# Kernel optimization log

Hardware: AMD Instinct MI355X
Metric: run time of the kernel (lower is better)

The kernel has to match this reference:

```python
import jax, jax.numpy as jnp
import numpy as np

B, S, D, H = 8, 1024, 1024, 16
HD = D // H  # head dim = 64


def setup_inputs() -> dict:
    key = jax.random.key(0)
    ks = jax.random.split(key, 8)
    return {
        "hidden_states": jax.random.normal(ks[0], (B, S, D), dtype=jnp.float32),
        "attention_mask": jnp.zeros((B, 1, 1, S), dtype=jnp.float32),
        "Wq": jax.random.normal(ks[1], (D, D), dtype=jnp.float32) * (1.0 / np.sqrt(D)),
        "bq": jax.random.normal(ks[2], (D,), dtype=jnp.float32) * 0.02,
        "Wk": jax.random.normal(ks[3], (D, D), dtype=jnp.float32) * (1.0 / np.sqrt(D)),
        "bk": jax.random.normal(ks[4], (D,), dtype=jnp.float32) * 0.02,
        "Wv": jax.random.normal(ks[5], (D, D), dtype=jnp.float32) * (1.0 / np.sqrt(D)),
        "bv": jax.random.normal(ks[6], (D,), dtype=jnp.float32) * 0.02,
    }


def _split_heads(x):
    # [B,S,D] -> [B,H,S,HD]
    return x.reshape(B, S, H, HD).transpose(0, 2, 1, 3)


def reference(hidden_states, attention_mask, Wq, bq, Wk, bk, Wv, bv):
    q = _split_heads(hidden_states @ Wq + bq)
    k = _split_heads(hidden_states @ Wk + bk)
    v = _split_heads(hidden_states @ Wv + bv)
    # [B,H,S,S]
    scores = jnp.einsum("bhqd,bhkd->bhqk", q, k) / jnp.sqrt(jnp.float32(HD))
    scores = scores + attention_mask
    probs = jax.nn.softmax(scores, axis=-1)  # dropout p=0.0 (eval)
    ctx = jnp.einsum("bhqk,bhkd->bhqd", probs, v)
    # [B,H,S,HD] -> [B,S,D]
    return ctx.transpose(0, 2, 1, 3).reshape(B, S, D)
```

## Files before the change

### kernel.cpp

```cpp
#include <hip/hip_runtime.h>
#include <stdint.h>

#define BB 8
#define SS 1024
#define DD 1024
#define HH 16
#define HDIM 64

typedef __bf16 bf16x8 __attribute__((ext_vector_type(8)));
typedef float f32x4 __attribute__((ext_vector_type(4)));

__device__ __forceinline__ unsigned short f2bf(float f) {
    union { float f; unsigned u; } v; v.f = f;
    unsigned r = v.u + 0x7fff + ((v.u >> 16) & 1);
    return (unsigned short)(r >> 16);
}

__device__ __forceinline__ float exp2fast(float x) {
#if __has_builtin(__builtin_amdgcn_exp2f)
    return __builtin_amdgcn_exp2f(x);
#else
    return __expf(x * 0.69314718f);
#endif
}

__device__ __forceinline__ void async16(void* lds, const void* g) {
    __builtin_amdgcn_global_load_lds(
        (const __attribute__((address_space(1))) unsigned int*)g,
        (__attribute__((address_space(3))) unsigned int*)lds, 16, 0, 0);
}

__global__ __launch_bounds__(256) void prep(
    const float* __restrict__ x, unsigned short* __restrict__ xb,
    const float* __restrict__ w0, const float* __restrict__ w1,
    const float* __restrict__ w2,
    unsigned short* __restrict__ f0, unsigned short* __restrict__ f1,
    unsigned short* __restrict__ f2)
{
    int bid = blockIdx.x;
    int tid = threadIdx.x;
    if (bid < 4096) {
        size_t base = ((size_t)bid << 11) + tid * 8;
        float4 v0 = *reinterpret_cast<const float4*>(x + base);
        float4 v1 = *reinterpret_cast<const float4*>(x + base + 4);
        union { unsigned short u16[8]; uint4 v; } o;
        o.u16[0] = f2bf(v0.x); o.u16[1] = f2bf(v0.y);
        o.u16[2] = f2bf(v0.z); o.u16[3] = f2bf(v0.w);
        o.u16[4] = f2bf(v1.x); o.u16[5] = f2bf(v1.y);
        o.u16[6] = f2bf(v1.z); o.u16[7] = f2bf(v1.w);
        *reinterpret_cast<uint4*>(xb + base) = o.v;
        return;
    }
    __shared__ unsigned short tile[64 * 76];
    int idx = bid - 4096;
    int z = idx >> 8, rem = idx & 255;
    const float* w = (z == 0) ? w0 : (z == 1) ? w1 : w2;
    unsigned short* wf = (z == 0) ? f0 : (z == 1) ? f1 : f2;
    int kt = rem & 15, nt = rem >> 4;
    const float* src = w + (size_t)(kt * 64) * DD + nt * 64;
    #pragma unroll
    for (int i = 0; i < 4; ++i) {
        int f = tid + i * 256;
        int r = f >> 4, c4 = f & 15;
        float4 v = *reinterpret_cast<const float4*>(src + r * DD + c4 * 4);
        ushort4 o;
        o.x = f2bf(v.x); o.y = f2bf(v.y); o.z = f2bf(v.z); o.w = f2bf(v.w);
        *reinterpret_cast<ushort4*>(&tile[r * 76 + c4 * 4]) = o;
    }
    __syncthreads();
    #pragma unroll
    for (int i = 0; i < 2; ++i) {
        int s = tid + i * 256;
        int r = s >> 3, c8 = s & 7;
        unsigned short tmp[8];
        #pragma unroll
        for (int j = 0; j < 8; ++j) tmp[j] = tile[(c8 * 8 + j) * 76 + r];
        *reinterpret_cast<uint4*>(wf + (size_t)(nt * 64 + r) * DD + kt * 64 + c8 * 8) =
            *reinterpret_cast<const uint4*>(tmp);
    }
}

__global__ __launch_bounds__(256, 2) void gemm_qkv(
    const unsigned short* __restrict__ xb,
    const unsigned short* __restrict__ wt0, const unsigned short* __restrict__ wt1,
    const unsigned short* __restrict__ wt2,
    const float* __restrict__ b0, const float* __restrict__ b1, const float* __restrict__ b2,
    unsigned short* __restrict__ qo, unsigned short* __restrict__ ko,
    unsigned short* __restrict__ vto)
{
    __shared__ unsigned short SH[32768];

    int bid = blockIdx.x;
    int xcd = bid & 7, g = bid >> 3;
    int strip = xcd * 3 + (g % 3);
    int mt = g / 3;
    int nt = strip & 7, z = strip >> 3;

    const unsigned short* wt; const float* bias; unsigned short* out;
    if (z == 0)      { wt = wt0; bias = b0; out = qo; }
    else if (z == 1) { wt = wt1; bias = b1; out = ko; }
    else             { wt = wt2; bias = b2; out = vto; }

    int tid = threadIdx.x;
    int wave = tid >> 6, lane = tid & 63, lq = lane >> 4, lm = lane & 15;
    int wr = wave >> 1, wc = wave & 1;

    const unsigned short* sA[4]; const unsigned short* sB[4];
    int dOff[4];
    #pragma unroll
    for (int s = 0; s < 4; ++s) {
        int o = tid + s * 256;
        int rw = o >> 3, cs = o & 7;
        int cl = (cs - rw) & 7;
        dOff[s] = o * 8;
        sA[s] = xb + (size_t)(mt * 128 + rw) * DD + cl * 8;
        sB[s] = wt + (size_t)(nt * 128 + rw) * DD + cl * 8;
    }

#define STAGE(P, KT)                                                          \
    {                                                                         \
        _Pragma("unroll") for (int s_ = 0; s_ < 4; ++s_)                      \
            async16(&SH[(P) * 8192 + dOff[s_]], sA[s_] + (KT) * 64);          \
        _Pragma("unroll") for (int s_ = 0; s_ < 4; ++s_)                      \
            async16(&SH[16384 + (P) * 8192 + dOff[s_]], sB[s_] + (KT) * 64);  \
    }

    int rA[4][2], rB[4][2];
    #pragma unroll
    for (int i = 0; i < 4; ++i) {
        int rwA = wr * 64 + i * 16 + lm;
        int rwB = wc * 64 + i * 16 + lm;
        #pragma unroll
        for (int ks = 0; ks < 2; ++ks) {
            rA[i][ks] = rwA * 64 + (((ks * 4 + lq) + rwA) & 7) * 8;
            rB[i][ks] = rwB * 64 + (((ks * 4 + lq) + rwB) & 7) * 8;
        }
    }

    f32x4 acc[4][4] = {};

#define COMPUTE(P)                                                            \
    {                                                                         \
        const unsigned short* Abuf = &SH[(P) * 8192];                         \
        const unsigned short* Bbuf = &SH[16384 + (P) * 8192];                 \
        _Pragma("unroll") for (int ks_ = 0; ks_ < 2; ++ks_) {                 \
            bf16x8 af[4], bf[4];                                              \
            _Pragma("unroll") for (int i_ = 0; i_ < 4; ++i_)                  \
                af[i_] = *reinterpret_cast<const bf16x8*>(Abuf + rA[i_][ks_]);\
            _Pragma("unroll") for (int j_ = 0; j_ < 4; ++j_)                  \
                bf[j_] = *reinterpret_cast<const bf16x8*>(Bbuf + rB[j_][ks_]);\
            _Pragma("unroll") for (int i_ = 0; i_ < 4; ++i_)                  \
                _Pragma("unroll") for (int j_ = 0; j_ < 4; ++j_)              \
                    acc[i_][j_] = __builtin_amdgcn_mfma_f32_16x16x32_bf16(    \
                        af[i_], bf[j_], acc[i_][j_], 0, 0, 0);                \
        }                                                                     \
    }

    STAGE(0, 0);
    STAGE(1, 1);

    for (int kt = 0; kt < 14; ++kt) {
        int p = kt & 1;
        asm volatile("s_waitcnt vmcnt(8)" ::: "memory");
        __builtin_amdgcn_s_barrier();
        __builtin_amdgcn_sched_barrier(0);
        COMPUTE(p);
        asm volatile("s_waitcnt lgkmcnt(0)" ::: "memory");
        __builtin_amdgcn_sched_barrier(0);
        __builtin_amdgcn_s_barrier();
        STAGE(p, kt + 2);
    }
    asm volatile("s_waitcnt vmcnt(8)" ::: "memory");
    __builtin_amdgcn_s_barrier();
    __builtin_amdgcn_sched_barrier(0);
    COMPUTE(0);
    asm volatile("s_waitcnt vmcnt(0)" ::: "memory");
    __builtin_amdgcn_s_barrier();
    __builtin_amdgcn_sched_barrier(0);
    COMPUTE(1);
#undef STAGE
#undef COMPUTE

    __syncthreads();

    int m0 = mt * 128;
    int col0 = nt * 128 + wc * 64;
    if (z == 2) {
        #pragma unroll
        for (int j = 0; j < 4; ++j) {
            int col = col0 + j * 16 + lm;
            float bsv = bias[col];
            int h = col >> 6, hd = col & 63;
            #pragma unroll
            for (int i = 0; i < 4; ++i) {
                int m = m0 + wr * 64 + i * 16 + lq * 4;
                int b_ = m >> 10, sr = m & 1023;
                union { float f; unsigned u; } p0, p1, p2, p3;
                p0.f = acc[i][j][0] + bsv; p1.f = acc[i][j][1] + bsv;
                p2.f = acc[i][j][2] + bsv; p3.f = acc[i][j][3] + bsv;
                uint2 pk;
                pk.x = __builtin_amdgcn_perm(p1.u + 0x8000u, p0.u + 0x8000u, 0x07060302u);
                pk.y = __builtin_amdgcn_perm(p3.u + 0x8000u, p2.u + 0x8000u, 0x07060302u);
                *reinterpret_cast<uint2*>(out + (((b_ * HH + h) * HDIM + hd) << 10) + sr) = pk;
            }
        }
    } else {
        unsigned short* S = SH + wave * 4864;
        #pragma unroll
        for (int j = 0; j < 4; ++j) {
            float bsv = bias[col0 + j * 16 + lm];
            #pragma unroll
            for (int i = 0; i < 4; ++i) {
                #pragma unroll
                for (int r = 0; r < 4; ++r) {
                    union { float f; unsigned u; } cv; cv.f = acc[i][j][r] + bsv;
                    S[(i * 16 + lq * 4 + r) * 76 + j * 16 + lm] =
                        (unsigned short)((cv.u + 0x8000u) >> 16);
                }
            }
        }
        int h = col0 >> 6;
        int mrow = m0 + wr * 64;
        int b_ = mrow >> 10, sr0 = mrow & 1023;
        unsigned short* ob = out + ((size_t)((b_ * HH + h) << 10) + sr0) * HDIM;
        #pragma unroll
        for (int u = 0; u < 8; ++u) {
            int s = lane + u * 64;
            int row = s >> 3, c8 = s & 7;
            uint4 v = *reinterpret_cast<const uint4*>(&S[row * 76 + c8 * 8]);
            *reinterpret_cast<uint4*>(ob + row * HDIM + c8 * 8) = v;
        }
    }
}

__global__ __launch_bounds__(256, 4) void attention(
    const unsigned short* __restrict__ q,
    const unsigned short* __restrict__ k,
    const unsigned short* __restrict__ vt,
    const float* __restrict__ mask,
    float* __restrict__ out)
{
    __shared__ unsigned short Ks[2][64 * 64];
    __shared__ unsigned short Vs[2][64 * 64];
    __shared__ unsigned short Ps[4][16 * 64];

    int blk = blockIdx.x;
    int xcd = blk & 7, j = blk >> 3;
    int bh = (xcd << 4) + (j >> 3);
    int qt = j & 7;
    int b = bh >> 4, h = bh & 15;

    int tid = threadIdx.x;
    int wave = tid >> 6, lane = tid & 63, lq = lane >> 4, lm = lane & 15;

    const unsigned short* qp = q + (size_t)bh * SS * HDIM;
    const unsigned short* kp = k + (size_t)bh * SS * HDIM;
    const unsigned short* vp = vt + (size_t)bh * HDIM * SS;
    const float* maskb = mask + b * SS;

    int qbase = qt * 128 + wave * 16 + lm;
    bf16x8 qa00 = *reinterpret_cast<const bf16x8*>(qp + qbase * HDIM + lq * 8);
    bf16x8 qa01 = *reinterpret_cast<const bf16x8*>(qp + qbase * HDIM + 32 + lq * 8);
    bf16x8 qa10 = *reinterpret_cast<const bf16x8*>(qp + (qbase + 64) * HDIM + lq * 8);
    bf16x8 qa11 = *reinterpret_cast<const bf16x8*>(qp + (qbase + 64) * HDIM + 32 + lq * 8);

    float lsum0 = 0.f, lsum1 = 0.f;
    f32x4 o0[4] = {}, o1[4] = {};

    int row0 = tid >> 3, sg = tid & 7;
    int cg = (sg - row0) & 7;
    const unsigned short* gk = kp + row0 * 64 + cg * 8;
    const unsigned short* gv = vp + row0 * SS + cg * 8;

    int sl0 = ((lq + lm) & 7) * 8;
    int sl1 = ((lq + lm + 4) & 7) * 8;
    unsigned short* Pw = Ps[wave];
    int pwbase = lm * 64 + (lq & 1) * 4;
    int prd0 = lm * 64 + sl0;
    int prd1 = lm * 64 + sl1;

    async16(&Ks[0][tid * 8], gk);  async16(&Ks[0][(tid + 256) * 8], gk + 32 * 64);
    async16(&Vs[0][tid * 8], gv);  async16(&Vs[0][(tid + 256) * 8], gv + 32 * SS);
    gk += 64 * 64; gv += 64;

    for (int t = 0; t < 16; ++t) {
        int p = t & 1;
        __syncthreads();
        int kb0 = t * 64;

        float4 mk[4];
        #pragma unroll
        for (int nb = 0; nb < 4; ++nb) {
            mk[nb] = *reinterpret_cast<const float4*>(maskb + kb0 + nb * 16 + lq * 4);
            #pragma unroll
            for (int r = 0; r < 4; ++r)
                reinterpret_cast<float*>(&mk[nb])[r] *= 1.44269504f;
        }
        if (t < 15) {
            async16(&Ks[p ^ 1][tid * 8], gk);  async16(&Ks[p ^ 1][(tid + 256) * 8], gk + 32 * 64);
            async16(&Vs[p ^ 1][tid * 8], gv);  async16(&Vs[p ^ 1][(tid + 256) * 8], gv + 32 * SS);
            gk += 64 * 64; gv += 64;
        }

        f32x4 c0[4], c1[4];
        #pragma unroll
        for (int nb = 0; nb < 4; ++nb) {
            bf16x8 kf0 = *reinterpret_cast<const bf16x8*>(&Ks[p][(nb * 16 + lm) * 64 + sl0]);
            bf16x8 kf1 = *reinterpret_cast<const bf16x8*>(&Ks[p][(nb * 16 + lm) * 64 + sl1]);
            f32x4 z = {};
            z = __builtin_amdgcn_mfma_f32_16x16x32_bf16(kf0, qa00, z, 0, 0, 0);
            z = __builtin_amdgcn_mfma_f32_16x16x32_bf16(kf1, qa01, z, 0, 0, 0);
            c0[nb] = z;
            f32x4 w = {};
            w = __builtin_amdgcn_mfma_f32_16x16x32_bf16(kf0, qa10, w, 0, 0, 0);
            w = __builtin_amdgcn_mfma_f32_16x16x32_bf16(kf1, qa11, w, 0, 0, 0);
            c1[nb] = w;
        }

        #pragma unroll
        for (int nb = 0; nb < 4; ++nb) {
            unsigned u[4];
            #pragma unroll
            for (int r = 0; r < 4; ++r) {
                float e = exp2fast(fmaf(c0[nb][r], 0.18033688f,
                                        reinterpret_cast<const float*>(&mk[nb])[r]));
                union { float f; unsigned v; } cv; cv.f = e;
                u[r] = cv.v;
                union { unsigned v; float f; } tr; tr.v = cv.v & 0xffff0000u;
                lsum0 += tr.f;
            }
            uint2 pk;
            pk.x = __builtin_amdgcn_perm(u[1], u[0], 0x07060302u);
            pk.y = __builtin_amdgcn_perm(u[3], u[2], 0x07060302u);
            *reinterpret_cast<uint2*>(
                &Pw[pwbase + (((nb * 2 + (lq >> 1)) + lm) & 7) * 8]) = pk;
        }
        bf16x8 pa00 = *reinterpret_cast<const bf16x8*>(&Pw[prd0]);
        bf16x8 pa01 = *reinterpret_cast<const bf16x8*>(&Pw[prd1]);

        #pragma unroll
        for (int nb = 0; nb < 4; ++nb) {
            unsigned u[4];
            #pragma unroll
            for (int r = 0; r < 4; ++r) {
                float e = exp2fast(fmaf(c1[nb][r], 0.18033688f,
                                        reinterpret_cast<const float*>(&mk[nb])[r]));
                union { float f; unsigned v; } cv; cv.f = e;
                u[r] = cv.v;
                union { unsigned v; float f; } tr; tr.v = cv.v & 0xffff0000u;
                lsum1 += tr.f;
            }
            uint2 pk;
            pk.x = __builtin_amdgcn_perm(u[1], u[0], 0x07060302u);
            pk.y = __builtin_amdgcn_perm(u[3], u[2], 0x07060302u);
            *reinterpret_cast<uint2*>(
                &Pw[pwbase + (((nb * 2 + (lq >> 1)) + lm) & 7) * 8]) = pk;
        }
        bf16x8 pa10 = *reinterpret_cast<const bf16x8*>(&Pw[prd0]);
        bf16x8 pa11 = *reinterpret_cast<const bf16x8*>(&Pw[prd1]);

        #pragma unroll
        for (int nb2 = 0; nb2 < 4; ++nb2) {
            bf16x8 vf0 = *reinterpret_cast<const bf16x8*>(&Vs[p][(nb2 * 16 + lm) * 64 + sl0]);
            o0[nb2] = __builtin_amdgcn_mfma_f32_16x16x32_bf16(pa00, vf0, o0[nb2], 0, 0, 0);
            o1[nb2] = __builtin_amdgcn_mfma_f32_16x16x32_bf16(pa10, vf0, o1[nb2], 0, 0, 0);
            bf16x8 vf1 = *reinterpret_cast<const bf16x8*>(&Vs[p][(nb2 * 16 + lm) * 64 + sl1]);
            o0[nb2] = __builtin_amdgcn_mfma_f32_16x16x32_bf16(pa01, vf1, o0[nb2], 0, 0, 0);
            o1[nb2] = __builtin_amdgcn_mfma_f32_16x16x32_bf16(pa11, vf1, o1[nb2], 0, 0, 0);
        }
    }

    lsum0 += __shfl_xor(lsum0, 16, 64);
    lsum0 += __shfl_xor(lsum0, 32, 64);
    lsum1 += __shfl_xor(lsum1, 16, 64);
    lsum1 += __shfl_xor(lsum1, 32, 64);
    float linv0[4], linv1[4];
    #pragma unroll
    for (int r = 0; r < 4; ++r) {
        linv0[r] = 1.0f / __shfl(lsum0, lq * 4 + r, 64);
        linv1[r] = 1.0f / __shfl(lsum1, lq * 4 + r, 64);
    }

    int srb = qt * 128 + wave * 16;
    #pragma unroll
    for (int nb2 = 0; nb2 < 4; ++nb2) {
        #pragma unroll
        for (int r = 0; r < 4; ++r) {
            int sr = srb + lq * 4 + r;
            out[((size_t)(b * SS + sr)) * DD + h * HDIM + nb2 * 16 + lm] =
                o0[nb2][r] * linv0[r];
            out[((size_t)(b * SS + sr + 64)) * DD + h * HDIM + nb2 * 16 + lm] =
                o1[nb2][r] * linv1[r];
        }
    }
}

extern "C" void kernel_launch(void* const* d_in, const int* in_sizes, int n_in,
                              void* d_out, int out_size, void* d_ws, size_t ws_size,
                              hipStream_t stream) {
    const float* hs   = (const float*)d_in[0];
    const float* mask = (const float*)d_in[1];
    const float* Wq   = (const float*)d_in[2];
    const float* bq   = (const float*)d_in[3];
    const float* Wk   = (const float*)d_in[4];
    const float* bk   = (const float*)d_in[5];
    const float* Wv   = (const float*)d_in[6];
    const float* bv   = (const float*)d_in[7];
    float* out = (float*)d_out;

    char* ws = (char*)d_ws;
    unsigned short* XB  = (unsigned short*)(ws);
    unsigned short* WT0 = (unsigned short*)(ws + 16777216);
    unsigned short* WT1 = (unsigned short*)(ws + 18874368);
    unsigned short* WT2 = (unsigned short*)(ws + 20971520);
    unsigned short* qw  = (unsigned short*)(ws + 23068672);
    unsigned short* kw  = (unsigned short*)(ws + 39845888);
    unsigned short* vtw = (unsigned short*)(ws + 56623104);

    prep<<<4864, 256, 0, stream>>>(hs, XB, Wq, Wk, Wv, WT0, WT1, WT2);
    gemm_qkv<<<1536, 256, 0, stream>>>(XB, WT0, WT1, WT2,
                                       bq, bk, bv, qw, kw, vtw);
    attention<<<1024, 256, 0, stream>>>(qw, kw, vtw, mask, out);
}
```

Baseline: 216.8 us.

## Enlarge QKV GEMM tile to 256x128 with 8 waves and software-pipelined LDS reads

The QKV projection GEMM moves from 256-thread 128x128 tiles to 512-thread 256x128 tiles, halving the grid and sharing each staged B tile across twice as many rows. The inner loop is split into quadrant steps: LDS fragment reads for the next quadrant are double-buffered in registers and overlap MFMA work. The next global-to-LDS stage is issued mid-tile, and wave priority is raised around MFMA bursts. The aim is less global and LDS traffic per FLOP and less stall between LDS reads and matrix ops. The cost is more barriers, higher register and LDS use (96 KB) with one block per CU, and fewer blocks to balance across CUs.

```diff
diff --git a/kernel.cpp b/kernel.cpp
--- a/kernel.cpp
+++ b/kernel.cpp
@@ -29,6 +29,15 @@
         (const __attribute__((address_space(1))) unsigned int*)g,
         (__attribute__((address_space(3))) unsigned int*)lds, 16, 0, 0);
 }
+
+#define WAITVM6 asm volatile("s_waitcnt vmcnt(6)" ::: "memory")
+#define WAITVM0 asm volatile("s_waitcnt vmcnt(0)" ::: "memory")
+#define WAITLG8 asm volatile("s_waitcnt lgkmcnt(8)" ::: "memory")
+#define WAITLG0 asm volatile("s_waitcnt lgkmcnt(0)" ::: "memory")
+#define SB0 __builtin_amdgcn_sched_barrier(0)
+#define BAR __builtin_amdgcn_s_barrier()
+#define PRIO1 __builtin_amdgcn_s_setprio(1)
+#define PRIO0 __builtin_amdgcn_s_setprio(0)
 
 __global__ __launch_bounds__(256) void prep(
     const float* __restrict__ x, unsigned short* __restrict__ xb,
@@ -80,7 +89,7 @@
     }
 }
 
-__global__ __launch_bounds__(256, 2) void gemm_qkv(
+__global__ __launch_bounds__(512, 1) void gemm_qkv(
     const unsigned short* __restrict__ xb,
     const unsigned short* __restrict__ wt0, const unsigned short* __restrict__ wt1,
     const unsigned short* __restrict__ wt2,
@@ -88,7 +97,7 @@
     unsigned short* __restrict__ qo, unsigned short* __restrict__ ko,
     unsigned short* __restrict__ vto)
 {
-    __shared__ unsigned short SH[32768];
+    __shared__ unsigned short SH[49152];
 
     int bid = blockIdx.x;
     int xcd = bid & 7, g = bid >> 3;
@@ -105,24 +114,31 @@
     int wave = tid >> 6, lane = tid & 63, lq = lane >> 4, lm = lane & 15;
     int wr = wave >> 1, wc = wave & 1;
 
-    const unsigned short* sA[4]; const unsigned short* sB[4];
-    int dOff[4];
+    const unsigned short* gA[4]; const unsigned short* gB[2];
+    int dA[4], dB[2];
     #pragma unroll
     for (int s = 0; s < 4; ++s) {
-        int o = tid + s * 256;
+        int o = tid + s * 512;
         int rw = o >> 3, cs = o & 7;
         int cl = (cs - rw) & 7;
-        dOff[s] = o * 8;
-        sA[s] = xb + (size_t)(mt * 128 + rw) * DD + cl * 8;
-        sB[s] = wt + (size_t)(nt * 128 + rw) * DD + cl * 8;
+        dA[s] = o * 8;
+        gA[s] = xb + (size_t)(mt * 256 + rw) * DD + cl * 8;
+    }
+    #pragma unroll
+    for (int s = 0; s < 2; ++s) {
+        int o = tid + s * 512;
+        int rw = o >> 3, cs = o & 7;
+        int cl = (cs - rw) & 7;
+        dB[s] = o * 8;
+        gB[s] = wt + (size_t)(nt * 128 + rw) * DD + cl * 8;
     }
 
 #define STAGE(P, KT)                                                          \
     {                                                                         \
         _Pragma("unroll") for (int s_ = 0; s_ < 4; ++s_)                      \
-            async16(&SH[(P) * 8192 + dOff[s_]], sA[s_] + (KT) * 64);          \
-        _Pragma("unroll") for (int s_ = 0; s_ < 4; ++s_)                      \
-            async16(&SH[16384 + (P) * 8192 + dOff[s_]], sB[s_] + (KT) * 64);  \
+            async16(&SH[(P) * 16384 + dA[s_]], gA[s_] + (KT) * 64);           \
+        _Pragma("unroll") for (int s_ = 0; s_ < 2; ++s_)                      \
+            async16(&SH[32768 + (P) * 8192 + dB[s_]], gB[s_] + (KT) * 64);    \
     }
 
     int rA[4][2], rB[4][2];
@@ -138,52 +154,98 @@
     }
 
     f32x4 acc[4][4] = {};
-
-#define COMPUTE(P)                                                            \
+    bf16x8 aR[2][2][2], bR[2][2][2];
+
+#define DSREAD(SET, QI, QJ, AB, BBp)                                          \
     {                                                                         \
-        const unsigned short* Abuf = &SH[(P) * 8192];                         \
-        const unsigned short* Bbuf = &SH[16384 + (P) * 8192];                 \
-        _Pragma("unroll") for (int ks_ = 0; ks_ < 2; ++ks_) {                 \
-            bf16x8 af[4], bf[4];                                              \
-            _Pragma("unroll") for (int i_ = 0; i_ < 4; ++i_)                  \
-                af[i_] = *reinterpret_cast<const bf16x8*>(Abuf + rA[i_][ks_]);\
-            _Pragma("unroll") for (int j_ = 0; j_ < 4; ++j_)                  \
-                bf[j_] = *reinterpret_cast<const bf16x8*>(Bbuf + rB[j_][ks_]);\
-            _Pragma("unroll") for (int i_ = 0; i_ < 4; ++i_)                  \
-                _Pragma("unroll") for (int j_ = 0; j_ < 4; ++j_)              \
-                    acc[i_][j_] = __builtin_amdgcn_mfma_f32_16x16x32_bf16(    \
-                        af[i_], bf[j_], acc[i_][j_], 0, 0, 0);                \
-        }                                                                     \
+        _Pragma("unroll") for (int ii_ = 0; ii_ < 2; ++ii_)                   \
+        _Pragma("unroll") for (int ks_ = 0; ks_ < 2; ++ks_)                   \
+            aR[SET][ii_][ks_] = *reinterpret_cast<const bf16x8*>(             \
+                (AB) + rA[(QI) * 2 + ii_][ks_]);                              \
+        _Pragma("unroll") for (int jj_ = 0; jj_ < 2; ++jj_)                   \
+        _Pragma("unroll") for (int ks_ = 0; ks_ < 2; ++ks_)                   \
+            bR[SET][jj_][ks_] = *reinterpret_cast<const bf16x8*>(             \
+                (BBp) + rB[(QJ) * 2 + jj_][ks_]);                             \
+    }
+#define MFMAQ(SET, QI, QJ)                                                    \
+    {                                                                         \
+        _Pragma("unroll") for (int ks_ = 0; ks_ < 2; ++ks_)                   \
+        _Pragma("unroll") for (int ii_ = 0; ii_ < 2; ++ii_)                   \
+        _Pragma("unroll") for (int jj_ = 0; jj_ < 2; ++jj_)                   \
+            acc[(QI) * 2 + ii_][(QJ) * 2 + jj_] =                             \
+                __builtin_amdgcn_mfma_f32_16x16x32_bf16(                      \
+                    aR[SET][ii_][ks_], bR[SET][jj_][ks_],                     \
+                    acc[(QI) * 2 + ii_][(QJ) * 2 + jj_], 0, 0, 0);            \
+    }
+
+#define TILE_STEADY(P, KT)                                                    \
+    {                                                                         \
+        const unsigned short* Ab  = &SH[(P) * 16384];                         \
+        const unsigned short* Bb  = &SH[32768 + (P) * 8192];                  \
+        const unsigned short* AbN = &SH[((P) ^ 1) * 16384];                   \
+        const unsigned short* BbN = &SH[32768 + ((P) ^ 1) * 8192];            \
+        DSREAD(1, 0, 1, Ab, Bb); BAR; WAITLG8; SB0;                           \
+        PRIO1; MFMAQ(0, 0, 0); PRIO0;                                         \
+        DSREAD(0, 1, 0, Ab, Bb); BAR; WAITLG8; SB0;                           \
+        PRIO1; MFMAQ(1, 0, 1); PRIO0;                                         \
+        DSREAD(1, 1, 1, Ab, Bb); BAR; WAITLG8; SB0;                           \
+        PRIO1; MFMAQ(0, 1, 0); PRIO0;                                         \
+        WAITLG0; SB0; BAR;                  \
+        STAGE(P, (KT) + 2);                   \
+        PRIO1; MFMAQ(1, 1, 1); PRIO0;                 \
+        WAITVM6; BAR; SB0;                   \
+        DSREAD(0, 0, 0, AbN, BbN);                       \
     }
 
     STAGE(0, 0);
     STAGE(1, 1);
-
-    for (int kt = 0; kt < 14; ++kt) {
-        int p = kt & 1;
-        asm volatile("s_waitcnt vmcnt(8)" ::: "memory");
-        __builtin_amdgcn_s_barrier();
-        __builtin_amdgcn_sched_barrier(0);
-        COMPUTE(p);
-        asm volatile("s_waitcnt lgkmcnt(0)" ::: "memory");
-        __builtin_amdgcn_sched_barrier(0);
-        __builtin_amdgcn_s_barrier();
-        STAGE(p, kt + 2);
-    }
-    asm volatile("s_waitcnt vmcnt(8)" ::: "memory");
-    __builtin_amdgcn_s_barrier();
-    __builtin_amdgcn_sched_barrier(0);
-    COMPUTE(0);
-    asm volatile("s_waitcnt vmcnt(0)" ::: "memory");
-    __builtin_amdgcn_s_barrier();
-    __builtin_amdgcn_sched_barrier(0);
-    COMPUTE(1);
+    WAITVM6; BAR; SB0;
+    {
+        const unsigned short* Ab = &SH[0];
+        const unsigned short* Bb = &SH[32768];
+        DSREAD(0, 0, 0, Ab, Bb);
+    }
+
+    for (int kt = 0; kt < 14; kt += 2) {
+        TILE_STEADY(0, kt);
+        TILE_STEADY(1, kt + 1);
+    }
+    {
+        const unsigned short* Ab  = &SH[0];
+        const unsigned short* Bb  = &SH[32768];
+        const unsigned short* AbN = &SH[16384];
+        const unsigned short* BbN = &SH[40960];
+        DSREAD(1, 0, 1, Ab, Bb); BAR; WAITLG8; SB0;
+        PRIO1; MFMAQ(0, 0, 0); PRIO0;
+        DSREAD(0, 1, 0, Ab, Bb); BAR; WAITLG8; SB0;
+        PRIO1; MFMAQ(1, 0, 1); PRIO0;
+        DSREAD(1, 1, 1, Ab, Bb); BAR; WAITLG8; SB0;
+        PRIO1; MFMAQ(0, 1, 0); PRIO0;
+        WAITLG0; SB0; BAR;
+        PRIO1; MFMAQ(1, 1, 1); PRIO0;
+        WAITVM0; BAR; SB0;
+        DSREAD(0, 0, 0, AbN, BbN);
+    }
+    {
+        const unsigned short* Ab = &SH[16384];
+        const unsigned short* Bb = &SH[40960];
+        DSREAD(1, 0, 1, Ab, Bb); BAR; WAITLG8; SB0;
+        PRIO1; MFMAQ(0, 0, 0); PRIO0;
+        DSREAD(0, 1, 0, Ab, Bb); BAR; WAITLG8; SB0;
+        PRIO1; MFMAQ(1, 0, 1); PRIO0;
+        DSREAD(1, 1, 1, Ab, Bb); BAR; WAITLG8; SB0;
+        PRIO1; MFMAQ(0, 1, 0); PRIO0;
+        WAITLG0; SB0;
+        PRIO1; MFMAQ(1, 1, 1); PRIO0;
+    }
+#undef TILE_STEADY
+#undef DSREAD
+#undef MFMAQ
 #undef STAGE
-#undef COMPUTE
 
     __syncthreads();
 
-    int m0 = mt * 128;
+    int m0 = mt * 256;
     int col0 = nt * 128 + wc * 64;
     if (z == 2) {
         #pragma unroll
@@ -418,7 +480,7 @@
     unsigned short* vtw = (unsigned short*)(ws + 56623104);
 
     prep<<<4864, 256, 0, stream>>>(hs, XB, Wq, Wk, Wv, WT0, WT1, WT2);
-    gemm_qkv<<<1536, 256, 0, stream>>>(XB, WT0, WT1, WT2,
-                                       bq, bk, bv, qw, kw, vtw);
+    gemm_qkv<<<768, 512, 0, stream>>>(XB, WT0, WT1, WT2,
+                                      bq, bk, bv, qw, kw, vtw);
     attention<<<1024, 256, 0, stream>>>(qw, kw, vtw, mask, out);
 }
```

Result: slower. 221.6 us (+2.2%).

## Enlarge QKV GEMM tiles to 256x256 with 8 waves and phased pipeline

Applied to the files above, without the earlier changes.

The QKV projection GEMM moves from 128x128 tiles with 4 waves to 256x256 tiles with 8 waves, using 128KB of LDS and 384 blocks. The main loop is split into four phases that interleave LDS fragment reads, async global-to-LDS prefetch of the next k-tile's halves, and MFMA bursts raised with s_setprio. The aim is higher arithmetic intensity per byte loaded and better overlap of loads with MFMA work. The trade-off is fewer blocks than CUs (384 on a 256-CU part gives a partial second wave), higher register pressure from the 8x4 accumulators, and more barriers per k-step.

```diff
diff --git a/kernel.cpp b/kernel.cpp
--- a/kernel.cpp
+++ b/kernel.cpp
@@ -29,6 +29,13 @@
         (const __attribute__((address_space(1))) unsigned int*)g,
         (__attribute__((address_space(3))) unsigned int*)lds, 16, 0, 0);
 }
+
+#define WAITVM0 asm volatile("s_waitcnt vmcnt(0)" ::: "memory")
+#define WAITLG0 asm volatile("s_waitcnt lgkmcnt(0)" ::: "memory")
+#define SB0 __builtin_amdgcn_sched_barrier(0)
+#define BAR __builtin_amdgcn_s_barrier()
+#define PRIO1 __builtin_amdgcn_s_setprio(1)
+#define PRIO0 __builtin_amdgcn_s_setprio(0)
 
 __global__ __launch_bounds__(256) void prep(
     const float* __restrict__ x, unsigned short* __restrict__ xb,
@@ -80,7 +87,7 @@
     }
 }
 
-__global__ __launch_bounds__(256, 2) void gemm_qkv(
+__global__ __launch_bounds__(512, 2) void gemm_qkv(
     const unsigned short* __restrict__ xb,
     const unsigned short* __restrict__ wt0, const unsigned short* __restrict__ wt1,
     const unsigned short* __restrict__ wt2,
@@ -88,13 +95,14 @@
     unsigned short* __restrict__ qo, unsigned short* __restrict__ ko,
     unsigned short* __restrict__ vto)
 {
-    __shared__ unsigned short SH[32768];
+    __shared__ unsigned short SH[65536];
 
     int bid = blockIdx.x;
     int xcd = bid & 7, g = bid >> 3;
-    int strip = xcd * 3 + (g % 3);
-    int mt = g / 3;
-    int nt = strip & 7, z = strip >> 3;
+    int lin = xcd * 48 + g;
+    int mt = lin & 31;
+    int strip = lin >> 5;
+    int nt = strip & 3, z = strip >> 2;
 
     const unsigned short* wt; const float* bias; unsigned short* out;
     if (z == 0)      { wt = wt0; bias = b0; out = qo; }
@@ -103,88 +111,91 @@
 
     int tid = threadIdx.x;
     int wave = tid >> 6, lane = tid & 63, lq = lane >> 4, lm = lane & 15;
-    int wr = wave >> 1, wc = wave & 1;
-
-    const unsigned short* sA[4]; const unsigned short* sB[4];
-    int dOff[4];
-    #pragma unroll
-    for (int s = 0; s < 4; ++s) {
-        int o = tid + s * 256;
-        int rw = o >> 3, cs = o & 7;
-        int cl = (cs - rw) & 7;
-        dOff[s] = o * 8;
-        sA[s] = xb + (size_t)(mt * 128 + rw) * DD + cl * 8;
-        sB[s] = wt + (size_t)(nt * 128 + rw) * DD + cl * 8;
-    }
-
-#define STAGE(P, KT)                                                          \
-    {                                                                         \
-        _Pragma("unroll") for (int s_ = 0; s_ < 4; ++s_)                      \
-            async16(&SH[(P) * 8192 + dOff[s_]], sA[s_] + (KT) * 64);          \
-        _Pragma("unroll") for (int s_ = 0; s_ < 4; ++s_)                      \
-            async16(&SH[16384 + (P) * 8192 + dOff[s_]], sB[s_] + (KT) * 64);  \
-    }
-
-    int rA[4][2], rB[4][2];
-    #pragma unroll
-    for (int i = 0; i < 4; ++i) {
-        int rwA = wr * 64 + i * 16 + lm;
-        int rwB = wc * 64 + i * 16 + lm;
-        #pragma unroll
-        for (int ks = 0; ks < 2; ++ks) {
-            rA[i][ks] = rwA * 64 + (((ks * 4 + lq) + rwA) & 7) * 8;
-            rB[i][ks] = rwB * 64 + (((ks * 4 + lq) + rwB) & 7) * 8;
-        }
-    }
-
-    f32x4 acc[4][4] = {};
-
-#define COMPUTE(P)                                                            \
-    {                                                                         \
-        const unsigned short* Abuf = &SH[(P) * 8192];                         \
-        const unsigned short* Bbuf = &SH[16384 + (P) * 8192];                 \
-        _Pragma("unroll") for (int ks_ = 0; ks_ < 2; ++ks_) {                 \
-            bf16x8 af[4], bf[4];                                              \
-            _Pragma("unroll") for (int i_ = 0; i_ < 4; ++i_)                  \
-                af[i_] = *reinterpret_cast<const bf16x8*>(Abuf + rA[i_][ks_]);\
-            _Pragma("unroll") for (int j_ = 0; j_ < 4; ++j_)                  \
-                bf[j_] = *reinterpret_cast<const bf16x8*>(Bbuf + rB[j_][ks_]);\
-            _Pragma("unroll") for (int i_ = 0; i_ < 4; ++i_)                  \
-                _Pragma("unroll") for (int j_ = 0; j_ < 4; ++j_)              \
-                    acc[i_][j_] = __builtin_amdgcn_mfma_f32_16x16x32_bf16(    \
-                        af[i_], bf[j_], acc[i_][j_], 0, 0, 0);                \
-        }                                                                     \
-    }
-
-    STAGE(0, 0);
-    STAGE(1, 1);
-
-    for (int kt = 0; kt < 14; ++kt) {
-        int p = kt & 1;
-        asm volatile("s_waitcnt vmcnt(8)" ::: "memory");
-        __builtin_amdgcn_s_barrier();
-        __builtin_amdgcn_sched_barrier(0);
-        COMPUTE(p);
-        asm volatile("s_waitcnt lgkmcnt(0)" ::: "memory");
-        __builtin_amdgcn_sched_barrier(0);
-        __builtin_amdgcn_s_barrier();
-        STAGE(p, kt + 2);
-    }
-    asm volatile("s_waitcnt vmcnt(8)" ::: "memory");
-    __builtin_amdgcn_s_barrier();
-    __builtin_amdgcn_sched_barrier(0);
-    COMPUTE(0);
-    asm volatile("s_waitcnt vmcnt(0)" ::: "memory");
-    __builtin_amdgcn_s_barrier();
-    __builtin_amdgcn_sched_barrier(0);
-    COMPUTE(1);
-#undef STAGE
-#undef COMPUTE
+    int wr = wave >> 2, wc = wave & 3;
+
+    const unsigned short *gA0, *gA1, *gB0, *gB1;
+    int d0, d1;
+    {
+        int o0 = tid,        rw0 = o0 >> 3, c0 = o0 & 7, cl0 = (c0 - rw0) & 7;
+        int o1 = tid + 512,  rw1 = o1 >> 3, c1 = o1 & 7, cl1 = (c1 - rw1) & 7;
+        d0 = o0 * 8; d1 = o1 * 8;
+        gA0 = xb + (size_t)(mt * 256 + rw0) * DD + cl0 * 8;
+        gA1 = xb + (size_t)(mt * 256 + rw1) * DD + cl1 * 8;
+        gB0 = wt + (size_t)(nt * 256 + rw0) * DD + cl0 * 8;
+        gB1 = wt + (size_t)(nt * 256 + rw1) * DD + cl1 * 8;
+    }
+
+#define STG_A(P, MH, KT)                                                       \
+    {                                                                          \
+        async16(&SH[(P) * 16384 + (MH) * 8192 + d0], gA0 + (MH) * 131072 + (KT) * 64); \
+        async16(&SH[(P) * 16384 + (MH) * 8192 + d1], gA1 + (MH) * 131072 + (KT) * 64); \
+    }
+#define STG_B(P, NH, KT)                                                       \
+    {                                                                          \
+        async16(&SH[32768 + (P) * 16384 + (NH) * 8192 + d0], gB0 + (NH) * 131072 + (KT) * 64); \
+        async16(&SH[32768 + (P) * 16384 + (NH) * 8192 + d1], gB1 + (NH) * 131072 + (KT) * 64); \
+    }
+
+    int s0 = ((lq + lm) & 7) * 8;
+    int s1 = ((lq + lm + 4) & 7) * 8;
+    int aRow = (wr * 128 + lm) * 64;
+    int bRow = (wc * 64 + lm) * 64;
+
+    f32x4 acc[8][4] = {};
+    bf16x8 af[4], bf[4];
+
+#define RDA(P, MH, SL)                                                         \
+    {                                                                          \
+        _Pragma("unroll") for (int ii_ = 0; ii_ < 4; ++ii_)                    \
+            af[ii_] = *reinterpret_cast<const bf16x8*>(                        \
+                SH + (P) * 16384 + aRow + (MH) * 4096 + ii_ * 1024 + (SL));    \
+    }
+#define RDB(P, SL)                                                             \
+    {                                                                          \
+        _Pragma("unroll") for (int jj_ = 0; jj_ < 4; ++jj_)                    \
+            bf[jj_] = *reinterpret_cast<const bf16x8*>(                        \
+                SH + 32768 + (P) * 16384 + bRow + jj_ * 1024 + (SL));          \
+    }
+#define MF(MH)                                                                 \
+    {                                                                          \
+        _Pragma("unroll") for (int jj_ = 0; jj_ < 4; ++jj_)                    \
+        _Pragma("unroll") for (int ii_ = 0; ii_ < 4; ++ii_)                    \
+            acc[(MH) * 4 + ii_][jj_] = __builtin_amdgcn_mfma_f32_16x16x32_bf16(\
+                af[ii_], bf[jj_], acc[(MH) * 4 + ii_][jj_], 0, 0, 0);          \
+    }
+
+#define PH0(P, T1, G) { RDA(P, 0, s0); RDB(P, s0); if (G) STG_A((P)^1, 0, T1); \
+                        BAR; WAITLG0; SB0; PRIO1; MF(0); PRIO0; BAR; }
+#define PH1(P, T1, G) { RDA(P, 1, s0);             if (G) STG_A((P)^1, 1, T1); \
+                        BAR; WAITLG0; SB0; PRIO1; MF(1); PRIO0; BAR; }
+#define PH2(P, T1, G) { RDA(P, 0, s1); RDB(P, s1); if (G) STG_B((P)^1, 0, T1); \
+                        BAR; WAITLG0; SB0; PRIO1; MF(0); PRIO0; BAR; }
+#define PH3(P, T1, G) { RDA(P, 1, s1);             if (G) STG_B((P)^1, 1, T1); \
+                        BAR; WAITLG0; SB0; PRIO1; MF(1); PRIO0; WAITVM0; BAR; }
+
+    STG_A(0, 0, 0); STG_A(0, 1, 0); STG_B(0, 0, 0); STG_B(0, 1, 0);
+    WAITVM0; BAR;
+
+    for (int t = 0; t < 16; t += 2) {
+        int t1 = t + 1, t2 = t + 2;
+        PH0(0, t1, 1); PH1(0, t1, 1); PH2(0, t1, 1); PH3(0, t1, 1);
+        int g2 = (t2 < 16);
+        PH0(1, t2, g2); PH1(1, t2, g2); PH2(1, t2, g2); PH3(1, t2, g2);
+    }
+#undef PH0
+#undef PH1
+#undef PH2
+#undef PH3
+#undef RDA
+#undef RDB
+#undef MF
+#undef STG_A
+#undef STG_B
 
     __syncthreads();
 
-    int m0 = mt * 128;
-    int col0 = nt * 128 + wc * 64;
+    int m0 = mt * 256;
+    int col0 = nt * 256 + wc * 64;
     if (z == 2) {
         #pragma unroll
         for (int j = 0; j < 4; ++j) {
@@ -192,8 +203,8 @@
             float bsv = bias[col];
             int h = col >> 6, hd = col & 63;
             #pragma unroll
-            for (int i = 0; i < 4; ++i) {
-                int m = m0 + wr * 64 + i * 16 + lq * 4;
+            for (int i = 0; i < 8; ++i) {
+                int m = m0 + wr * 128 + i * 16 + lq * 4;
                 int b_ = m >> 10, sr = m & 1023;
                 union { float f; unsigned u; } p0, p1, p2, p3;
                 p0.f = acc[i][j][0] + bsv; p1.f = acc[i][j][1] + bsv;
@@ -206,29 +217,33 @@
         }
     } else {
         unsigned short* S = SH + wave * 4864;
-        #pragma unroll
-        for (int j = 0; j < 4; ++j) {
-            float bsv = bias[col0 + j * 16 + lm];
-            #pragma unroll
-            for (int i = 0; i < 4; ++i) {
+        int h = col0 >> 6;
+        #pragma unroll
+        for (int h2 = 0; h2 < 2; ++h2) {
+            #pragma unroll
+            for (int j = 0; j < 4; ++j) {
+                float bsv = bias[col0 + j * 16 + lm];
                 #pragma unroll
-                for (int r = 0; r < 4; ++r) {
-                    union { float f; unsigned u; } cv; cv.f = acc[i][j][r] + bsv;
-                    S[(i * 16 + lq * 4 + r) * 76 + j * 16 + lm] =
-                        (unsigned short)((cv.u + 0x8000u) >> 16);
+                for (int i2 = 0; i2 < 4; ++i2) {
+                    int i = h2 * 4 + i2;
+                    #pragma unroll
+                    for (int r = 0; r < 4; ++r) {
+                        union { float f; unsigned u; } cv; cv.f = acc[i][j][r] + bsv;
+                        S[(i2 * 16 + lq * 4 + r) * 76 + j * 16 + lm] =
+                            (unsigned short)((cv.u + 0x8000u) >> 16);
+                    }
                 }
             }
-        }
-        int h = col0 >> 6;
-        int mrow = m0 + wr * 64;
-        int b_ = mrow >> 10, sr0 = mrow & 1023;
-        unsigned short* ob = out + ((size_t)((b_ * HH + h) << 10) + sr0) * HDIM;
-        #pragma unroll
-        for (int u = 0; u < 8; ++u) {
-            int s = lane + u * 64;
-            int row = s >> 3, c8 = s & 7;
-            uint4 v = *reinterpret_cast<const uint4*>(&S[row * 76 + c8 * 8]);
-            *reinterpret_cast<uint4*>(ob + row * HDIM + c8 * 8) = v;
+            int mrow = m0 + wr * 128 + h2 * 64;
+            int b_ = mrow >> 10, sr0 = mrow & 1023;
+            unsigned short* ob = out + ((size_t)((b_ * HH + h) << 10) + sr0) * HDIM;
+            #pragma unroll
+            for (int u = 0; u < 8; ++u) {
+                int s = lane + u * 64;
+                int row = s >> 3, c8 = s & 7;
+                uint4 v = *reinterpret_cast<const uint4*>(&S[row * 76 + c8 * 8]);
+                *reinterpret_cast<uint4*>(ob + row * HDIM + c8 * 8) = v;
+            }
         }
     }
 }
@@ -418,7 +433,7 @@
     unsigned short* vtw = (unsigned short*)(ws + 56623104);
 
     prep<<<4864, 256, 0, stream>>>(hs, XB, Wq, Wk, Wv, WT0, WT1, WT2);
-    gemm_qkv<<<1536, 256, 0, stream>>>(XB, WT0, WT1, WT2,
-                                       bq, bk, bv, qw, kw, vtw);
+    gemm_qkv<<<384, 512, 0, stream>>>(XB, WT0, WT1, WT2,
+                                      bq, bk, bv, qw, kw, vtw);
     attention<<<1024, 256, 0, stream>>>(qw, kw, vtw, mask, out);
 }
```

Result: slower. 225.9 us (+4.2%).

## Process 256 query rows per attention block to double K/V tile reuse

Applied to the files above, without the earlier changes.

Each attention workgroup now handles 256 query rows (four 64-row sub-tiles per wave) instead of 128, so every K/V tile staged in LDS is reused across twice as many queries and global K/V traffic is halved. The grid shrinks to 512 blocks and launch bounds drop to 2 blocks per CU to make room for the larger accumulator and score register arrays. The cost is higher register pressure, lower occupancy and fewer blocks to spread across CUs, which may leave some CUs idle or limit latency hiding.

```diff
diff --git a/kernel.cpp b/kernel.cpp
--- a/kernel.cpp
+++ b/kernel.cpp
@@ -233,7 +233,7 @@
     }
 }
 
-__global__ __launch_bounds__(256, 4) void attention(
+__global__ __launch_bounds__(256, 2) void attention(
     const unsigned short* __restrict__ q,
     const unsigned short* __restrict__ k,
     const unsigned short* __restrict__ vt,
@@ -246,8 +246,8 @@
 
     int blk = blockIdx.x;
     int xcd = blk & 7, j = blk >> 3;
-    int bh = (xcd << 4) + (j >> 3);
-    int qt = j & 7;
+    int bh = (xcd << 4) + (j >> 2);
+    int qt = j & 3;
     int b = bh >> 4, h = bh & 15;
 
     int tid = threadIdx.x;
@@ -258,14 +258,16 @@
     const unsigned short* vp = vt + (size_t)bh * HDIM * SS;
     const float* maskb = mask + b * SS;
 
-    int qbase = qt * 128 + wave * 16 + lm;
-    bf16x8 qa00 = *reinterpret_cast<const bf16x8*>(qp + qbase * HDIM + lq * 8);
-    bf16x8 qa01 = *reinterpret_cast<const bf16x8*>(qp + qbase * HDIM + 32 + lq * 8);
-    bf16x8 qa10 = *reinterpret_cast<const bf16x8*>(qp + (qbase + 64) * HDIM + lq * 8);
-    bf16x8 qa11 = *reinterpret_cast<const bf16x8*>(qp + (qbase + 64) * HDIM + 32 + lq * 8);
-
-    float lsum0 = 0.f, lsum1 = 0.f;
-    f32x4 o0[4] = {}, o1[4] = {};
+    int qbase = qt * 256 + wave * 16 + lm;
+    bf16x8 qa[4][2];
+    #pragma unroll
+    for (int s = 0; s < 4; ++s) {
+        qa[s][0] = *reinterpret_cast<const bf16x8*>(qp + (qbase + s * 64) * HDIM + lq * 8);
+        qa[s][1] = *reinterpret_cast<const bf16x8*>(qp + (qbase + s * 64) * HDIM + 32 + lq * 8);
+    }
+
+    float lsum[4] = {0.f, 0.f, 0.f, 0.f};
+    f32x4 o[4][4] = {};
 
     int row0 = tid >> 3, sg = tid & 7;
     int cg = (sg - row0) & 7;
@@ -302,95 +304,78 @@
             gk += 64 * 64; gv += 64;
         }
 
-        f32x4 c0[4], c1[4];
+        f32x4 c[4][4];
         #pragma unroll
         for (int nb = 0; nb < 4; ++nb) {
             bf16x8 kf0 = *reinterpret_cast<const bf16x8*>(&Ks[p][(nb * 16 + lm) * 64 + sl0]);
             bf16x8 kf1 = *reinterpret_cast<const bf16x8*>(&Ks[p][(nb * 16 + lm) * 64 + sl1]);
-            f32x4 z = {};
-            z = __builtin_amdgcn_mfma_f32_16x16x32_bf16(kf0, qa00, z, 0, 0, 0);
-            z = __builtin_amdgcn_mfma_f32_16x16x32_bf16(kf1, qa01, z, 0, 0, 0);
-            c0[nb] = z;
-            f32x4 w = {};
-            w = __builtin_amdgcn_mfma_f32_16x16x32_bf16(kf0, qa10, w, 0, 0, 0);
-            w = __builtin_amdgcn_mfma_f32_16x16x32_bf16(kf1, qa11, w, 0, 0, 0);
-            c1[nb] = w;
-        }
-
-        #pragma unroll
-        for (int nb = 0; nb < 4; ++nb) {
-            unsigned u[4];
-            #pragma unroll
-            for (int r = 0; r < 4; ++r) {
-                float e = exp2fast(fmaf(c0[nb][r], 0.18033688f,
-                                        reinterpret_cast<const float*>(&mk[nb])[r]));
-                union { float f; unsigned v; } cv; cv.f = e;
-                u[r] = cv.v;
-                union { unsigned v; float f; } tr; tr.v = cv.v & 0xffff0000u;
-                lsum0 += tr.f;
-            }
-            uint2 pk;
-            pk.x = __builtin_amdgcn_perm(u[1], u[0], 0x07060302u);
-            pk.y = __builtin_amdgcn_perm(u[3], u[2], 0x07060302u);
-            *reinterpret_cast<uint2*>(
-                &Pw[pwbase + (((nb * 2 + (lq >> 1)) + lm) & 7) * 8]) = pk;
-        }
-        bf16x8 pa00 = *reinterpret_cast<const bf16x8*>(&Pw[prd0]);
-        bf16x8 pa01 = *reinterpret_cast<const bf16x8*>(&Pw[prd1]);
-
-        #pragma unroll
-        for (int nb = 0; nb < 4; ++nb) {
-            unsigned u[4];
-            #pragma unroll
-            for (int r = 0; r < 4; ++r) {
-                float e = exp2fast(fmaf(c1[nb][r], 0.18033688f,
-                                        reinterpret_cast<const float*>(&mk[nb])[r]));
-                union { float f; unsigned v; } cv; cv.f = e;
-                u[r] = cv.v;
-                union { unsigned v; float f; } tr; tr.v = cv.v & 0xffff0000u;
-                lsum1 += tr.f;
-            }
-            uint2 pk;
-            pk.x = __builtin_amdgcn_perm(u[1], u[0], 0x07060302u);
-            pk.y = __builtin_amdgcn_perm(u[3], u[2], 0x07060302u);
-            *reinterpret_cast<uint2*>(
-                &Pw[pwbase + (((nb * 2 + (lq >> 1)) + lm) & 7) * 8]) = pk;
-        }
-        bf16x8 pa10 = *reinterpret_cast<const bf16x8*>(&Pw[prd0]);
-        bf16x8 pa11 = *reinterpret_cast<const bf16x8*>(&Pw[prd1]);
+            #pragma unroll
+            for (int s = 0; s < 4; ++s) {
+                f32x4 z = {};
+                z = __builtin_amdgcn_mfma_f32_16x16x32_bf16(kf0, qa[s][0], z, 0, 0, 0);
+                z = __builtin_amdgcn_mfma_f32_16x16x32_bf16(kf1, qa[s][1], z, 0, 0, 0);
+                c[s][nb] = z;
+            }
+        }
+
+        bf16x8 pa[4][2];
+        #pragma unroll
+        for (int s = 0; s < 4; ++s) {
+            #pragma unroll
+            for (int nb = 0; nb < 4; ++nb) {
+                unsigned u[4];
+                #pragma unroll
+                for (int r = 0; r < 4; ++r) {
+                    float e = exp2fast(fmaf(c[s][nb][r], 0.18033688f,
+                                            reinterpret_cast<const float*>(&mk[nb])[r]));
+                    union { float f; unsigned v; } cv; cv.f = e;
+                    u[r] = cv.v;
+                    union { unsigned v; float f; } tr; tr.v = cv.v & 0xffff0000u;
+                    lsum[s] += tr.f;
+                }
+                uint2 pk;
+                pk.x = __builtin_amdgcn_perm(u[1], u[0], 0x07060302u);
+                pk.y = __builtin_amdgcn_perm(u[3], u[2], 0x07060302u);
+                *reinterpret_cast<uint2*>(
+                    &Pw[pwbase + (((nb * 2 + (lq >> 1)) + lm) & 7) * 8]) = pk;
+            }
+            pa[s][0] = *reinterpret_cast<const bf16x8*>(&Pw[prd0]);
+            pa[s][1] = *reinterpret_cast<const bf16x8*>(&Pw[prd1]);
+        }
 
         #pragma unroll
         for (int nb2 = 0; nb2 < 4; ++nb2) {
             bf16x8 vf0 = *reinterpret_cast<const bf16x8*>(&Vs[p][(nb2 * 16 + lm) * 64 + sl0]);
-            o0[nb2] = __builtin_amdgcn_mfma_f32_16x16x32_bf16(pa00, vf0, o0[nb2], 0, 0, 0);
-            o1[nb2] = __builtin_amdgcn_mfma_f32_16x16x32_bf16(pa10, vf0, o1[nb2], 0, 0, 0);
             bf16x8 vf1 = *reinterpret_cast<const bf16x8*>(&Vs[p][(nb2 * 16 + lm) * 64 + sl1]);
-            o0[nb2] = __builtin_amdgcn_mfma_f32_16x16x32_bf16(pa01, vf1, o0[nb2], 0, 0, 0);
-            o1[nb2] = __builtin_amdgcn_mfma_f32_16x16x32_bf16(pa11, vf1, o1[nb2], 0, 0, 0);
-        }
-    }
-
-    lsum0 += __shfl_xor(lsum0, 16, 64);
-    lsum0 += __shfl_xor(lsum0, 32, 64);
-    lsum1 += __shfl_xor(lsum1, 16, 64);
-    lsum1 += __shfl_xor(lsum1, 32, 64);
-    float linv0[4], linv1[4];
-    #pragma unroll
-    for (int r = 0; r < 4; ++r) {
-        linv0[r] = 1.0f / __shfl(lsum0, lq * 4 + r, 64);
-        linv1[r] = 1.0f / __shfl(lsum1, lq * 4 + r, 64);
-    }
-
-    int srb = qt * 128 + wave * 16;
-    #pragma unroll
-    for (int nb2 = 0; nb2 < 4; ++nb2) {
-        #pragma unroll
-        for (int r = 0; r < 4; ++r) {
-            int sr = srb + lq * 4 + r;
-            out[((size_t)(b * SS + sr)) * DD + h * HDIM + nb2 * 16 + lm] =
-                o0[nb2][r] * linv0[r];
-            out[((size_t)(b * SS + sr + 64)) * DD + h * HDIM + nb2 * 16 + lm] =
-                o1[nb2][r] * linv1[r];
+            #pragma unroll
+            for (int s = 0; s < 4; ++s) {
+                o[s][nb2] = __builtin_amdgcn_mfma_f32_16x16x32_bf16(pa[s][0], vf0, o[s][nb2], 0, 0, 0);
+                o[s][nb2] = __builtin_amdgcn_mfma_f32_16x16x32_bf16(pa[s][1], vf1, o[s][nb2], 0, 0, 0);
+            }
+        }
+    }
+
+    float linv[4][4];
+    #pragma unroll
+    for (int s = 0; s < 4; ++s) {
+        lsum[s] += __shfl_xor(lsum[s], 16, 64);
+        lsum[s] += __shfl_xor(lsum[s], 32, 64);
+        #pragma unroll
+        for (int r = 0; r < 4; ++r)
+            linv[s][r] = 1.0f / __shfl(lsum[s], lq * 4 + r, 64);
+    }
+
+    int srb = qt * 256 + wave * 16;
+    #pragma unroll
+    for (int s = 0; s < 4; ++s) {
+        #pragma unroll
+        for (int nb2 = 0; nb2 < 4; ++nb2) {
+            #pragma unroll
+            for (int r = 0; r < 4; ++r) {
+                int sr = srb + s * 64 + lq * 4 + r;
+                out[((size_t)(b * SS + sr)) * DD + h * HDIM + nb2 * 16 + lm] =
+                    o[s][nb2][r] * linv[s][r];
+            }
         }
     }
 }
@@ -420,5 +405,5 @@
     prep<<<4864, 256, 0, stream>>>(hs, XB, Wq, Wk, Wv, WT0, WT1, WT2);
     gemm_qkv<<<1536, 256, 0, stream>>>(XB, WT0, WT1, WT2,
                                        bq, bk, bv, qw, kw, vtw);
-    attention<<<1024, 256, 0, stream>>>(qw, kw, vtw, mask, out);
-}
+    attention<<<512, 256, 0, stream>>>(qw, kw, vtw, mask, out);
+}
```

Result: faster. 210.4 us (median of 2 runs) (-3.0%).
